# Optimization experiments

Measured on AMD Instinct MI355X. Metric: run time of the kernel, lower is better.

## Reference

```python
import jax, jax.numpy as jnp
import numpy as np

EPS = 1e-5


def conv1x1(x, w, b):
    # x: [b,c,h,w], w: [o,c], b: [o] -> [b,o,h,w]  (1x1 conv == channel matmul)
    return jnp.einsum('bchw,oc->bohw', x, w) + b[None, :, None, None]


def nor_mean_std(x):
    # instance norm over spatial dims (torch calc_mean_std uses unbiased var)
    mean = jnp.mean(x, axis=(2, 3), keepdims=True)
    var = jnp.var(x, axis=(2, 3), keepdims=True, ddof=1)
    return (x - mean) / jnp.sqrt(var + EPS)


def nor_mean(x):
    mean = jnp.mean(x, axis=(2, 3), keepdims=True)
    return x - mean, mean


def net(x, w1, b1, w2, b2):
    return conv1x1(jax.nn.relu(conv1x1(x, w1, b1)), w2, b2)


def setup_inputs() -> dict:
    key = jax.random.key(0)
    ks = jax.random.split(key, 8)
    B, C, H, W = 8, 256, 128, 128
    return {
        'content': jax.random.normal(ks[0], (B, C, H, W), jnp.float32),
        'style': jax.random.normal(ks[1], (B, C, H, W), jnp.float32),
        'w1': jax.random.normal(ks[2], (128, 256), jnp.float32) * 0.05,
        'b1': jax.random.normal(ks[3], (128,), jnp.float32) * 0.05,
        'w2': jax.random.normal(ks[4], (32, 128), jnp.float32) * 0.05,
        'b2': jax.random.normal(ks[5], (32,), jnp.float32) * 0.05,
        'wu': jax.random.normal(ks[6], (256, 32), jnp.float32) * 0.05,
        'bu': jax.random.normal(ks[7], (256,), jnp.float32) * 0.05,
    }


def reference(content, style, w1, b1, w2, b2, wu, bu):
    cF_nor = nor_mean_std(content)
    sF_nor, smean = nor_mean(style)
    cF = net(cF_nor, w1, b1, w2, b2)          # [b,32,h,w]
    sF = net(sF_nor, w1, b1, w2, b2)          # [b,32,h,w]
    b, c, h, w = cF.shape
    hw = h * w
    sf = sF.reshape(b, c, hw)
    # channel covariance: [b,32,32]
    s_cov = jnp.einsum('bcn,bdn->bcd', sf, sf) / hw
    s_cov = jax.nn.softmax(s_cov, axis=-1) * (c ** -0.5)
    gF = jnp.einsum('bcd,bdn->bcn', s_cov, cF.reshape(b, c, hw)).reshape(b, c, h, w)
    gF = conv1x1(gF, wu, bu)                  # [b,256,h,w]
    return gF + smean + content
```

## Files before the change

### kernel.cpp

```cpp
#include <hip/hip_runtime.h>

#define HW 16384
#define C_IN 256
#define C_MID 128
#define C_OUT 32
#define EPSF 1e-5f

typedef __bf16 bf16x8 __attribute__((ext_vector_type(8)));
typedef __bf16 bf16x4 __attribute__((ext_vector_type(4)));
typedef float f32x4 __attribute__((ext_vector_type(4)));

__global__ __launch_bounds__(512) void k_stats6(const float* __restrict__ content,
                                                const float* __restrict__ style,
                                                float* __restrict__ cmean,
                                                float* __restrict__ crstd,
                                                float* __restrict__ smean) {
    const int bc = blockIdx.x;
    const int t = threadIdx.x;
    const f32x4* cp = (const f32x4*)(content + (size_t)bc * HW);
    const f32x4* sp = (const f32x4*)(style + (size_t)bc * HW);
    const int phase = (bc * 257) & 4095;

    f32x4 c0 = __builtin_nontemporal_load(cp + ((phase + t          ) & 4095));
    f32x4 c1 = __builtin_nontemporal_load(cp + ((phase + t +  1*512) & 4095));
    f32x4 c2 = __builtin_nontemporal_load(cp + ((phase + t +  2*512) & 4095));
    f32x4 c3 = __builtin_nontemporal_load(cp + ((phase + t +  3*512) & 4095));
    f32x4 c4 = __builtin_nontemporal_load(cp + ((phase + t +  4*512) & 4095));
    f32x4 c5 = __builtin_nontemporal_load(cp + ((phase + t +  5*512) & 4095));
    f32x4 c6 = __builtin_nontemporal_load(cp + ((phase + t +  6*512) & 4095));
    f32x4 c7 = __builtin_nontemporal_load(cp + ((phase + t +  7*512) & 4095));
    f32x4 s0 = __builtin_nontemporal_load(sp + ((phase + t          ) & 4095));
    f32x4 s1 = __builtin_nontemporal_load(sp + ((phase + t +  1*512) & 4095));
    f32x4 s2 = __builtin_nontemporal_load(sp + ((phase + t +  2*512) & 4095));
    f32x4 s3 = __builtin_nontemporal_load(sp + ((phase + t +  3*512) & 4095));
    f32x4 s4 = __builtin_nontemporal_load(sp + ((phase + t +  4*512) & 4095));
    f32x4 s5 = __builtin_nontemporal_load(sp + ((phase + t +  5*512) & 4095));
    f32x4 s6 = __builtin_nontemporal_load(sp + ((phase + t +  6*512) & 4095));
    f32x4 s7 = __builtin_nontemporal_load(sp + ((phase + t +  7*512) & 4095));
    asm volatile("" ::
        "v"(c0), "v"(c1), "v"(c2), "v"(c3), "v"(c4), "v"(c5), "v"(c6), "v"(c7),
        "v"(s0), "v"(s1), "v"(s2), "v"(s3), "v"(s4), "v"(s5), "v"(s6), "v"(s7));

    float cs, cq, ss;
    {
        f32x4 a01 = c0 + c1, a23 = c2 + c3, a45 = c4 + c5, a67 = c6 + c7;
        f32x4 a = (a01 + a23) + (a45 + a67);
        cs = (a[0] + a[1]) + (a[2] + a[3]);
        f32x4 q01 = c0 * c0 + c1 * c1, q23 = c2 * c2 + c3 * c3;
        f32x4 q45 = c4 * c4 + c5 * c5, q67 = c6 * c6 + c7 * c7;
        f32x4 q = (q01 + q23) + (q45 + q67);
        cq = (q[0] + q[1]) + (q[2] + q[3]);
        f32x4 b01 = s0 + s1, b23 = s2 + s3, b45 = s4 + s5, b67 = s6 + s7;
        f32x4 bsum = (b01 + b23) + (b45 + b67);
        ss = (bsum[0] + bsum[1]) + (bsum[2] + bsum[3]);
    }

    #pragma unroll
    for (int d = 32; d > 0; d >>= 1) {
        cs += __shfl_xor(cs, d, 64);
        cq += __shfl_xor(cq, d, 64);
        ss += __shfl_xor(ss, d, 64);
    }
    __shared__ float rs[8], rq[8], rss[8];
    const int wv = t >> 6;
    if ((t & 63) == 0) { rs[wv] = cs; rq[wv] = cq; rss[wv] = ss; }
    __syncthreads();
    if (t == 0) {
        float S = 0.f, Q = 0.f, SS = 0.f;
        #pragma unroll
        for (int i = 0; i < 8; ++i) { S += rs[i]; Q += rq[i]; SS += rss[i]; }
        float n = (float)HW;
        float var = (Q - S * S / n) / (n - 1.f);
        cmean[bc] = S / n;
        crstd[bc] = 1.f / sqrtf(var + EPSF);
        smean[bc] = SS / n;
    }
}

__global__ __launch_bounds__(256) void k_wprep(const float* __restrict__ w1,
                                               const float* __restrict__ b1,
                                               const float* __restrict__ cmean,
                                               const float* __restrict__ crstd,
                                               const float* __restrict__ smean,
                                               __bf16* __restrict__ W1c,
                                               float* __restrict__ bias1c,
                                               __bf16* __restrict__ W1s,
                                               float* __restrict__ bias1s) {
    int o = blockIdx.x, b = blockIdx.y, t = threadIdx.x;
    float w = w1[o * 256 + t];
    float r = crstd[b * 256 + t];
    float wc = w * r;
    W1c[((size_t)(b * 128 + o)) * 256 + t] = (__bf16)wc;
    if (b == 0) W1s[o * 256 + t] = (__bf16)w;
    float pc = wc * cmean[b * 256 + t];
    float ps = w * smean[b * 256 + t];
    __shared__ float rA[256], rB[256];
    rA[t] = pc; rB[t] = ps;
    __syncthreads();
    for (int off = 128; off > 0; off >>= 1) {
        if (t < off) { rA[t] += rA[t + off]; rB[t] += rB[t + off]; }
        __syncthreads();
    }
    if (t == 0) {
        bias1c[b * 128 + o] = b1[o] - rA[0];
        bias1s[b * 128 + o] = b1[o] - rB[0];
    }
}

__global__ __launch_bounds__(256) void k_w2prep(const float* __restrict__ w2,
                                                __bf16* __restrict__ W2b) {
    int i = blockIdx.x * 256 + threadIdx.x;
    if (i < 4096) W2b[i] = (__bf16)w2[i];
}

__global__ __launch_bounds__(256) void k_net_mfma(const float* __restrict__ x,
                                                  const __bf16* __restrict__ W1,
                                                  const float* __restrict__ bias1,
                                                  const __bf16* __restrict__ W2,
                                                  const float* __restrict__ b2,
                                                  float* __restrict__ outF,
                                                  int w1_per_batch) {
    __shared__ __bf16 Xl[64 * 256];
    __shared__ __bf16 Tl[64 * 128];
    const int tid = threadIdx.x;
    const int l = tid & 63, wv = tid >> 6;
    const int lr = l & 15, g = l >> 4;
    const int sw = (lr & 7) << 4;
    const int p0 = blockIdx.x * 64;
    const int b = blockIdx.y;
    const float* xb = x + (size_t)b * C_IN * HW;

    {
        const int p = wv * 16 + lr;
        const float* xp = xb + p0 + p;
        char* row = (char*)&Xl[p * 256];
        #pragma unroll 4
        for (int cc = 0; cc < 16; ++cc) {
            const int c = cc * 16 + g * 4;
            float f0 = xp[(size_t)(c + 0) * HW];
            float f1 = xp[(size_t)(c + 1) * HW];
            float f2 = xp[(size_t)(c + 2) * HW];
            float f3 = xp[(size_t)(c + 3) * HW];
            bf16x4 v;
            v[0] = (__bf16)f0; v[1] = (__bf16)f1; v[2] = (__bf16)f2; v[3] = (__bf16)f3;
            *(bf16x4*)(row + ((c * 2) ^ sw)) = v;
        }
    }
    __syncthreads();

    const f32x4 zero4 = {0.f, 0.f, 0.f, 0.f};
    f32x4 acc[2][4];
    #pragma unroll
    for (int mt = 0; mt < 2; ++mt)
        #pragma unroll
        for (int nt = 0; nt < 4; ++nt) acc[mt][nt] = zero4;

    const __bf16* W1b = W1 + (w1_per_batch ? ((size_t)b << 15) : 0);
    const __bf16* wrow0 = W1b + (size_t)(wv * 32 + lr) * 256 + g * 8;
    const __bf16* wrow1 = wrow0 + 16 * 256;

    #pragma unroll
    for (int kt = 0; kt < 8; ++kt) {
        bf16x8 a0 = *(const bf16x8*)(wrow0 + kt * 32);
        bf16x8 a1 = *(const bf16x8*)(wrow1 + kt * 32);
        #pragma unroll
        for (int nt = 0; nt < 4; ++nt) {
            const char* xrow = (const char*)&Xl[(nt * 16 + lr) * 256];
            bf16x8 bfr = *(const bf16x8*)(xrow + (((kt * 32 + g * 8) * 2) ^ sw));
            acc[0][nt] = __builtin_amdgcn_mfma_f32_16x16x32_bf16(a0, bfr, acc[0][nt], 0, 0, 0);
            acc[1][nt] = __builtin_amdgcn_mfma_f32_16x16x32_bf16(a1, bfr, acc[1][nt], 0, 0, 0);
        }
    }

    float4 bia[2];
    bia[0] = *(const float4*)&bias1[b * 128 + wv * 32 + g * 4];
    bia[1] = *(const float4*)&bias1[b * 128 + wv * 32 + 16 + g * 4];
    #pragma unroll
    for (int mt = 0; mt < 2; ++mt) {
        #pragma unroll
        for (int nt = 0; nt < 4; ++nt) {
            const int p = nt * 16 + lr;
            char* trow = (char*)&Tl[p * 128];
            const int ob = (wv * 32 + mt * 16 + g * 4) * 2;
            bf16x4 tv;
            tv[0] = (__bf16)fmaxf(acc[mt][nt][0] + bia[mt].x, 0.f);
            tv[1] = (__bf16)fmaxf(acc[mt][nt][1] + bia[mt].y, 0.f);
            tv[2] = (__bf16)fmaxf(acc[mt][nt][2] + bia[mt].z, 0.f);
            tv[3] = (__bf16)fmaxf(acc[mt][nt][3] + bia[mt].w, 0.f);
            *(bf16x4*)(trow + (ob ^ sw)) = tv;
        }
    }
    __syncthreads();

    f32x4 acc2[2];
    acc2[0] = zero4; acc2[1] = zero4;
    const int p = wv * 16 + lr;
    const char* trow = (const char*)&Tl[p * 128];
    const __bf16* w2r0 = W2 + (size_t)lr * 128 + g * 8;
    const __bf16* w2r1 = w2r0 + 16 * 128;
    #pragma unroll
    for (int kt = 0; kt < 4; ++kt) {
        bf16x8 bfr = *(const bf16x8*)(trow + (((kt * 32 + g * 8) * 2) ^ sw));
        bf16x8 a0 = *(const bf16x8*)(w2r0 + kt * 32);
        bf16x8 a1 = *(const bf16x8*)(w2r1 + kt * 32);
        acc2[0] = __builtin_amdgcn_mfma_f32_16x16x32_bf16(a0, bfr, acc2[0], 0, 0, 0);
        acc2[1] = __builtin_amdgcn_mfma_f32_16x16x32_bf16(a1, bfr, acc2[1], 0, 0, 0);
    }
    float4 bb0 = *(const float4*)&b2[g * 4];
    float4 bb1 = *(const float4*)&b2[16 + g * 4];
    float* ob = outF + (size_t)b * C_OUT * HW + p0 + p;
    const int o0 = g * 4;
    ob[(size_t)(o0 + 0) * HW] = acc2[0][0] + bb0.x;
    ob[(size_t)(o0 + 1) * HW] = acc2[0][1] + bb0.y;
    ob[(size_t)(o0 + 2) * HW] = acc2[0][2] + bb0.z;
    ob[(size_t)(o0 + 3) * HW] = acc2[0][3] + bb0.w;
    ob[(size_t)(16 + o0 + 0) * HW] = acc2[1][0] + bb1.x;
    ob[(size_t)(16 + o0 + 1) * HW] = acc2[1][1] + bb1.y;
    ob[(size_t)(16 + o0 + 2) * HW] = acc2[1][2] + bb1.z;
    ob[(size_t)(16 + o0 + 3) * HW] = acc2[1][3] + bb1.w;
}

__global__ __launch_bounds__(256) void k_gram(const float* __restrict__ sF,
                                              float* __restrict__ partial) {
    __shared__ float sS[32 * 257];
    int b = blockIdx.y, sl = blockIdx.x;
    int t = threadIdx.x;
    const float* base = sF + (size_t)b * C_OUT * HW + sl * 1024;
    int i = t >> 3, jb = (t & 7) * 4;
    float acc[4] = {0.f, 0.f, 0.f, 0.f};
    for (int ch = 0; ch < 4; ++ch) {
        __syncthreads();
        #pragma unroll
        for (int r = 0; r < 32; ++r)
            sS[r * 257 + t] = base[(size_t)r * HW + ch * 256 + t];
        __syncthreads();
        for (int n = 0; n < 256; ++n) {
            float si = sS[i * 257 + n];
            #pragma unroll
            for (int q = 0; q < 4; ++q)
                acc[q] = fmaf(si, sS[(jb + q) * 257 + n], acc[q]);
        }
    }
    float* dst = partial + ((size_t)(b * 16 + sl)) * 1024 + t * 4;
    #pragma unroll
    for (int q = 0; q < 4; ++q) dst[q] = acc[q];
}

__global__ __launch_bounds__(1024) void k_softmax(const float* __restrict__ partial,
                                                  float* __restrict__ scov) {
    int b = blockIdx.x;
    int j = threadIdx.x, i = threadIdx.y;
    float v = 0.f;
    #pragma unroll
    for (int s = 0; s < 16; ++s)
        v += partial[((size_t)(b * 16 + s)) * 1024 + i * 32 + j];
    v *= (1.f / (float)HW);
    float m = v;
    #pragma unroll
    for (int d = 16; d > 0; d >>= 1) m = fmaxf(m, __shfl_xor(m, d, 32));
    float e = expf(v - m);
    float sum = e;
    #pragma unroll
    for (int d = 16; d > 0; d >>= 1) sum += __shfl_xor(sum, d, 32);
    scov[(size_t)b * 1024 + i * 32 + j] = e / sum * 0.17677669529663687f;
}

__global__ __launch_bounds__(256) void k_final(const float* __restrict__ cF,
                                               const float* __restrict__ scov,
                                               const float* __restrict__ wu,
                                               const float* __restrict__ bu,
                                               const float* __restrict__ smean,
                                               const float* __restrict__ content,
                                               float* __restrict__ out) {
    __shared__ float sCov[1024];
    __shared__ float sC[32 * 64];
    __shared__ float sG[32 * 64];
    __shared__ float sWu[32 * 260];
    int t = threadIdx.x;
    int p0 = blockIdx.x * 64;
    int b = blockIdx.y;
    #pragma unroll
    for (int q = 0; q < 4; ++q) sCov[t + 256 * q] = scov[(size_t)b * 1024 + t + 256 * q];
    {
        int p = t & 63, rb = t >> 6;
        #pragma unroll
        for (int pass = 0; pass < 8; ++pass) {
            int r = pass * 4 + rb;
            sC[r * 64 + p] = cF[(size_t)b * C_OUT * HW + (size_t)r * HW + p0 + p];
        }
    }
    {
        int k = t & 31, ob = t >> 5;
        #pragma unroll
        for (int pass = 0; pass < 32; ++pass) {
            int o = pass * 8 + ob;
            sWu[k * 260 + o] = wu[o * 32 + k];
        }
    }
    __syncthreads();
    {
        int gp = t & 63, gib = (t >> 6) * 8;
        #pragma unroll
        for (int rr = 0; rr < 8; ++rr) {
            int gi = gib + rr;
            float a = 0.f;
            #pragma unroll
            for (int k = 0; k < 32; ++k)
                a = fmaf(sCov[gi * 32 + k], sC[k * 64 + gp], a);
            sG[gi * 64 + gp] = a;
        }
    }
    __syncthreads();
    int tx = t & 7, ty = t >> 3;
    float acc[8][8];
    #pragma unroll
    for (int i = 0; i < 8; ++i)
        #pragma unroll
        for (int j = 0; j < 8; ++j) acc[i][j] = 0.f;
    #pragma unroll 4
    for (int k = 0; k < 32; ++k) {
        float4 a4a = *(const float4*)&sWu[k * 260 + ty * 8];
        float4 a4b = *(const float4*)&sWu[k * 260 + ty * 8 + 4];
        float4 b4a = *(const float4*)&sG[k * 64 + tx * 8];
        float4 b4b = *(const float4*)&sG[k * 64 + tx * 8 + 4];
        float a[8] = {a4a.x, a4a.y, a4a.z, a4a.w, a4b.x, a4b.y, a4b.z, a4b.w};
        float bb[8] = {b4a.x, b4a.y, b4a.z, b4a.w, b4b.x, b4b.y, b4b.z, b4b.w};
        #pragma unroll
        for (int i = 0; i < 8; ++i)
            #pragma unroll
            for (int j = 0; j < 8; ++j)
                acc[i][j] = fmaf(a[i], bb[j], acc[i][j]);
    }
    #pragma unroll
    for (int i = 0; i < 8; ++i) {
        int o = ty * 8 + i;
        float add = bu[o] + smean[b * 256 + o];
        const float* csrc = content + (size_t)b * C_IN * HW + (size_t)o * HW + p0 + tx * 8;
        float* dst = out + (size_t)b * C_IN * HW + (size_t)o * HW + p0 + tx * 8;
        float4 c0 = *(const float4*)csrc;
        float4 c1 = *(const float4*)(csrc + 4);
        f32x4 r0 = {acc[i][0] + add + c0.x, acc[i][1] + add + c0.y,
                    acc[i][2] + add + c0.z, acc[i][3] + add + c0.w};
        f32x4 r1 = {acc[i][4] + add + c1.x, acc[i][5] + add + c1.y,
                    acc[i][6] + add + c1.z, acc[i][7] + add + c1.w};
        __builtin_nontemporal_store(r0, (f32x4*)dst);
        __builtin_nontemporal_store(r1, (f32x4*)(dst + 4));
    }
}

extern "C" void kernel_launch(void* const* d_in, const int* in_sizes, int n_in,
                              void* d_out, int out_size, void* d_ws, size_t ws_size,
                              hipStream_t stream) {
    const float* content = (const float*)d_in[0];
    const float* style   = (const float*)d_in[1];
    const float* w1      = (const float*)d_in[2];
    const float* b1      = (const float*)d_in[3];
    const float* w2      = (const float*)d_in[4];
    const float* b2      = (const float*)d_in[5];
    const float* wu      = (const float*)d_in[6];
    const float* bu      = (const float*)d_in[7];
    float* out = (float*)d_out;
    float* ws  = (float*)d_ws;

    float* cmean   = ws;
    float* crstd   = ws + 2048;
    float* smean   = ws + 4096;
    float* scov    = ws + 6144;
    __bf16* W2b    = (__bf16*)(ws + 6144);
    float* bias1c  = ws + 8192;
    float* bias1s  = ws + 9216;
    float* partial = ws + 14336;
    __bf16* W1c    = (__bf16*)(ws + 14336);
    __bf16* W1s    = (__bf16*)(ws + 145408);
    float* cF      = ws + 161792;
    float* sF      = cF + 4194304;

    k_stats6<<<dim3(2048), 512, 0, stream>>>(content, style, cmean, crstd, smean);
    k_wprep<<<dim3(128, 8), 256, 0, stream>>>(w1, b1, cmean, crstd, smean,
                                              W1c, bias1c, W1s, bias1s);
    k_w2prep<<<dim3(16), 256, 0, stream>>>(w2, W2b);
    k_net_mfma<<<dim3(256, 8), 256, 0, stream>>>(content, W1c, bias1c, W2b, b2, cF, 1);
    k_net_mfma<<<dim3(256, 8), 256, 0, stream>>>(style, W1s, bias1s, W2b, b2, sF, 0);
    k_gram<<<dim3(16, 8), 256, 0, stream>>>(sF, partial);
    k_softmax<<<dim3(8), dim3(32, 32), 0, stream>>>(partial, scov);
    k_final<<<dim3(256, 8), 256, 0, stream>>>(cF, scov, wu, bu, smean, content, out);
}
```

Measured before the change: 261.8 us.

## Emit bf16 input copies in stats pass and fuse gram into style net

The statistics kernel now also writes bf16 copies of content and style. Both net kernels read these half-width copies instead of the fp32 tensors. The style net computes per-block Gram partials directly from LDS, which removes the sF buffer and the separate gram kernel, and the softmax then reduces 256 partials instead of 16. The w2 conversion is merged into the weight-prep kernel, the final kernel reads Wu straight from global memory, and the residual content is read from the bf16 copy. Together these cut HBM traffic and launch count, at the cost of extra bf16 writes and lower precision on the residual add.

New measurement: 245.4 us. -6.3%, faster.

```diff
diff --git a/kernel.cpp b/kernel.cpp
--- a/kernel.cpp
+++ b/kernel.cpp
@@ -10,47 +10,59 @@
 typedef __bf16 bf16x4 __attribute__((ext_vector_type(4)));
 typedef float f32x4 __attribute__((ext_vector_type(4)));
 
-__global__ __launch_bounds__(512) void k_stats6(const float* __restrict__ content,
-                                                const float* __restrict__ style,
-                                                float* __restrict__ cmean,
-                                                float* __restrict__ crstd,
-                                                float* __restrict__ smean) {
+__device__ __forceinline__ bf16x4 cvt4(f32x4 v) {
+    bf16x4 r;
+    r[0] = (__bf16)v[0]; r[1] = (__bf16)v[1];
+    r[2] = (__bf16)v[2]; r[3] = (__bf16)v[3];
+    return r;
+}
+
+__global__ __launch_bounds__(512) void k_stats10(const float* __restrict__ content,
+                                                 const float* __restrict__ style,
+                                                 float* __restrict__ cmean,
+                                                 float* __restrict__ crstd,
+                                                 float* __restrict__ smean,
+                                                 __bf16* __restrict__ cbf,
+                                                 __bf16* __restrict__ sbf) {
     const int bc = blockIdx.x;
     const int t = threadIdx.x;
     const f32x4* cp = (const f32x4*)(content + (size_t)bc * HW);
     const f32x4* sp = (const f32x4*)(style + (size_t)bc * HW);
     const int phase = (bc * 257) & 4095;
 
-    f32x4 c0 = __builtin_nontemporal_load(cp + ((phase + t          ) & 4095));
-    f32x4 c1 = __builtin_nontemporal_load(cp + ((phase + t +  1*512) & 4095));
-    f32x4 c2 = __builtin_nontemporal_load(cp + ((phase + t +  2*512) & 4095));
-    f32x4 c3 = __builtin_nontemporal_load(cp + ((phase + t +  3*512) & 4095));
-    f32x4 c4 = __builtin_nontemporal_load(cp + ((phase + t +  4*512) & 4095));
-    f32x4 c5 = __builtin_nontemporal_load(cp + ((phase + t +  5*512) & 4095));
-    f32x4 c6 = __builtin_nontemporal_load(cp + ((phase + t +  6*512) & 4095));
-    f32x4 c7 = __builtin_nontemporal_load(cp + ((phase + t +  7*512) & 4095));
-    f32x4 s0 = __builtin_nontemporal_load(sp + ((phase + t          ) & 4095));
-    f32x4 s1 = __builtin_nontemporal_load(sp + ((phase + t +  1*512) & 4095));
-    f32x4 s2 = __builtin_nontemporal_load(sp + ((phase + t +  2*512) & 4095));
-    f32x4 s3 = __builtin_nontemporal_load(sp + ((phase + t +  3*512) & 4095));
-    f32x4 s4 = __builtin_nontemporal_load(sp + ((phase + t +  4*512) & 4095));
-    f32x4 s5 = __builtin_nontemporal_load(sp + ((phase + t +  5*512) & 4095));
-    f32x4 s6 = __builtin_nontemporal_load(sp + ((phase + t +  6*512) & 4095));
-    f32x4 s7 = __builtin_nontemporal_load(sp + ((phase + t +  7*512) & 4095));
+    int idx[8];
+    #pragma unroll
+    for (int i = 0; i < 8; ++i) idx[i] = (phase + t + i * 512) & 4095;
+
+    f32x4 c[8], s[8];
+    #pragma unroll
+    for (int i = 0; i < 8; ++i) c[i] = __builtin_nontemporal_load(cp + idx[i]);
+    #pragma unroll
+    for (int i = 0; i < 8; ++i) s[i] = __builtin_nontemporal_load(sp + idx[i]);
     asm volatile("" ::
-        "v"(c0), "v"(c1), "v"(c2), "v"(c3), "v"(c4), "v"(c5), "v"(c6), "v"(c7),
-        "v"(s0), "v"(s1), "v"(s2), "v"(s3), "v"(s4), "v"(s5), "v"(s6), "v"(s7));
+        "v"(c[0]), "v"(c[1]), "v"(c[2]), "v"(c[3]), "v"(c[4]), "v"(c[5]), "v"(c[6]), "v"(c[7]),
+        "v"(s[0]), "v"(s[1]), "v"(s[2]), "v"(s[3]), "v"(s[4]), "v"(s[5]), "v"(s[6]), "v"(s[7]));
+
+    {
+        bf16x4* cb = (bf16x4*)(cbf + (size_t)bc * HW);
+        bf16x4* sb = (bf16x4*)(sbf + (size_t)bc * HW);
+        #pragma unroll
+        for (int i = 0; i < 8; ++i) {
+            cb[idx[i]] = cvt4(c[i]);
+            sb[idx[i]] = cvt4(s[i]);
+        }
+    }
 
     float cs, cq, ss;
     {
-        f32x4 a01 = c0 + c1, a23 = c2 + c3, a45 = c4 + c5, a67 = c6 + c7;
+        f32x4 a01 = c[0] + c[1], a23 = c[2] + c[3], a45 = c[4] + c[5], a67 = c[6] + c[7];
         f32x4 a = (a01 + a23) + (a45 + a67);
         cs = (a[0] + a[1]) + (a[2] + a[3]);
-        f32x4 q01 = c0 * c0 + c1 * c1, q23 = c2 * c2 + c3 * c3;
-        f32x4 q45 = c4 * c4 + c5 * c5, q67 = c6 * c6 + c7 * c7;
+        f32x4 q01 = c[0]*c[0] + c[1]*c[1], q23 = c[2]*c[2] + c[3]*c[3];
+        f32x4 q45 = c[4]*c[4] + c[5]*c[5], q67 = c[6]*c[6] + c[7]*c[7];
         f32x4 q = (q01 + q23) + (q45 + q67);
         cq = (q[0] + q[1]) + (q[2] + q[3]);
-        f32x4 b01 = s0 + s1, b23 = s2 + s3, b45 = s4 + s5, b67 = s6 + s7;
+        f32x4 b01 = s[0] + s[1], b23 = s[2] + s[3], b45 = s[4] + s[5], b67 = s[6] + s[7];
         f32x4 bsum = (b01 + b23) + (b45 + b67);
         ss = (bsum[0] + bsum[1]) + (bsum[2] + bsum[3]);
     }
@@ -77,21 +89,26 @@
     }
 }
 
-__global__ __launch_bounds__(256) void k_wprep(const float* __restrict__ w1,
-                                               const float* __restrict__ b1,
-                                               const float* __restrict__ cmean,
-                                               const float* __restrict__ crstd,
-                                               const float* __restrict__ smean,
-                                               __bf16* __restrict__ W1c,
-                                               float* __restrict__ bias1c,
-                                               __bf16* __restrict__ W1s,
-                                               float* __restrict__ bias1s) {
+__global__ __launch_bounds__(256) void k_wprep2(const float* __restrict__ w1,
+                                                const float* __restrict__ b1,
+                                                const float* __restrict__ w2,
+                                                const float* __restrict__ cmean,
+                                                const float* __restrict__ crstd,
+                                                const float* __restrict__ smean,
+                                                __bf16* __restrict__ W1c,
+                                                float* __restrict__ bias1c,
+                                                __bf16* __restrict__ W1s,
+                                                float* __restrict__ bias1s,
+                                                __bf16* __restrict__ W2b) {
     int o = blockIdx.x, b = blockIdx.y, t = threadIdx.x;
     float w = w1[o * 256 + t];
     float r = crstd[b * 256 + t];
     float wc = w * r;
     W1c[((size_t)(b * 128 + o)) * 256 + t] = (__bf16)wc;
-    if (b == 0) W1s[o * 256 + t] = (__bf16)w;
+    if (b == 0) {
+        W1s[o * 256 + t] = (__bf16)w;
+        if (t < 32) W2b[o * 32 + t] = (__bf16)w2[o * 32 + t];
+    }
     float pc = wc * cmean[b * 256 + t];
     float ps = w * smean[b * 256 + t];
     __shared__ float rA[256], rB[256];
@@ -107,19 +124,15 @@
     }
 }
 
-__global__ __launch_bounds__(256) void k_w2prep(const float* __restrict__ w2,
-                                                __bf16* __restrict__ W2b) {
-    int i = blockIdx.x * 256 + threadIdx.x;
-    if (i < 4096) W2b[i] = (__bf16)w2[i];
-}
-
-__global__ __launch_bounds__(256) void k_net_mfma(const float* __restrict__ x,
-                                                  const __bf16* __restrict__ W1,
-                                                  const float* __restrict__ bias1,
-                                                  const __bf16* __restrict__ W2,
-                                                  const float* __restrict__ b2,
-                                                  float* __restrict__ outF,
-                                                  int w1_per_batch) {
+template <int MODE>
+__global__ __launch_bounds__(256) void k_net_bf(const __bf16* __restrict__ x,
+                                                const __bf16* __restrict__ W1,
+                                                const float* __restrict__ bias1,
+                                                const __bf16* __restrict__ W2,
+                                                const float* __restrict__ b2,
+                                                float* __restrict__ outF,
+                                                float* __restrict__ partial,
+                                                int w1_per_batch) {
     __shared__ __bf16 Xl[64 * 256];
     __shared__ __bf16 Tl[64 * 128];
     const int tid = threadIdx.x;
@@ -128,21 +141,20 @@
     const int sw = (lr & 7) << 4;
     const int p0 = blockIdx.x * 64;
     const int b = blockIdx.y;
-    const float* xb = x + (size_t)b * C_IN * HW;
+    const __bf16* xb = x + (size_t)b * C_IN * HW;
 
     {
         const int p = wv * 16 + lr;
-        const float* xp = xb + p0 + p;
+        const __bf16* xp = xb + p0 + p;
         char* row = (char*)&Xl[p * 256];
         #pragma unroll 4
         for (int cc = 0; cc < 16; ++cc) {
             const int c = cc * 16 + g * 4;
-            float f0 = xp[(size_t)(c + 0) * HW];
-            float f1 = xp[(size_t)(c + 1) * HW];
-            float f2 = xp[(size_t)(c + 2) * HW];
-            float f3 = xp[(size_t)(c + 3) * HW];
             bf16x4 v;
-            v[0] = (__bf16)f0; v[1] = (__bf16)f1; v[2] = (__bf16)f2; v[3] = (__bf16)f3;
+            v[0] = xp[(size_t)(c + 0) * HW];
+            v[1] = xp[(size_t)(c + 1) * HW];
+            v[2] = xp[(size_t)(c + 2) * HW];
+            v[3] = xp[(size_t)(c + 3) * HW];
             *(bf16x4*)(row + ((c * 2) ^ sw)) = v;
         }
     }
@@ -175,6 +187,7 @@
     float4 bia[2];
     bia[0] = *(const float4*)&bias1[b * 128 + wv * 32 + g * 4];
     bia[1] = *(const float4*)&bias1[b * 128 + wv * 32 + 16 + g * 4];
+    __syncthreads();
     #pragma unroll
     for (int mt = 0; mt < 2; ++mt) {
         #pragma unroll
@@ -208,53 +221,58 @@
     }
     float4 bb0 = *(const float4*)&b2[g * 4];
     float4 bb1 = *(const float4*)&b2[16 + g * 4];
-    float* ob = outF + (size_t)b * C_OUT * HW + p0 + p;
     const int o0 = g * 4;
-    ob[(size_t)(o0 + 0) * HW] = acc2[0][0] + bb0.x;
-    ob[(size_t)(o0 + 1) * HW] = acc2[0][1] + bb0.y;
-    ob[(size_t)(o0 + 2) * HW] = acc2[0][2] + bb0.z;
-    ob[(size_t)(o0 + 3) * HW] = acc2[0][3] + bb0.w;
-    ob[(size_t)(16 + o0 + 0) * HW] = acc2[1][0] + bb1.x;
-    ob[(size_t)(16 + o0 + 1) * HW] = acc2[1][1] + bb1.y;
-    ob[(size_t)(16 + o0 + 2) * HW] = acc2[1][2] + bb1.z;
-    ob[(size_t)(16 + o0 + 3) * HW] = acc2[1][3] + bb1.w;
-}
-
-__global__ __launch_bounds__(256) void k_gram(const float* __restrict__ sF,
-                                              float* __restrict__ partial) {
-    __shared__ float sS[32 * 257];
-    int b = blockIdx.y, sl = blockIdx.x;
-    int t = threadIdx.x;
-    const float* base = sF + (size_t)b * C_OUT * HW + sl * 1024;
-    int i = t >> 3, jb = (t & 7) * 4;
-    float acc[4] = {0.f, 0.f, 0.f, 0.f};
-    for (int ch = 0; ch < 4; ++ch) {
+
+    if constexpr (MODE == 0) {
+        float* ob = outF + (size_t)b * C_OUT * HW + p0 + p;
+        ob[(size_t)(o0 + 0) * HW] = acc2[0][0] + bb0.x;
+        ob[(size_t)(o0 + 1) * HW] = acc2[0][1] + bb0.y;
+        ob[(size_t)(o0 + 2) * HW] = acc2[0][2] + bb0.z;
+        ob[(size_t)(o0 + 3) * HW] = acc2[0][3] + bb0.w;
+        ob[(size_t)(16 + o0 + 0) * HW] = acc2[1][0] + bb1.x;
+        ob[(size_t)(16 + o0 + 1) * HW] = acc2[1][1] + bb1.y;
+        ob[(size_t)(16 + o0 + 2) * HW] = acc2[1][2] + bb1.z;
+        ob[(size_t)(16 + o0 + 3) * HW] = acc2[1][3] + bb1.w;
+    } else {
+        float* gt = (float*)Xl;
+        gt[(o0 + 0) * 65 + p] = acc2[0][0] + bb0.x;
+        gt[(o0 + 1) * 65 + p] = acc2[0][1] + bb0.y;
+        gt[(o0 + 2) * 65 + p] = acc2[0][2] + bb0.z;
+        gt[(o0 + 3) * 65 + p] = acc2[0][3] + bb0.w;
+        gt[(16 + o0 + 0) * 65 + p] = acc2[1][0] + bb1.x;
+        gt[(16 + o0 + 1) * 65 + p] = acc2[1][1] + bb1.y;
+        gt[(16 + o0 + 2) * 65 + p] = acc2[1][2] + bb1.z;
+        gt[(16 + o0 + 3) * 65 + p] = acc2[1][3] + bb1.w;
         __syncthreads();
-        #pragma unroll
-        for (int r = 0; r < 32; ++r)
-            sS[r * 257 + t] = base[(size_t)r * HW + ch * 256 + t];
-        __syncthreads();
-        for (int n = 0; n < 256; ++n) {
-            float si = sS[i * 257 + n];
+        const int gi = tid >> 3, jb = (tid & 7) * 4;
+        float g4[4] = {0.f, 0.f, 0.f, 0.f};
+        #pragma unroll 8
+        for (int n = 0; n < 64; ++n) {
+            float si = gt[gi * 65 + n];
             #pragma unroll
             for (int q = 0; q < 4; ++q)
-                acc[q] = fmaf(si, sS[(jb + q) * 257 + n], acc[q]);
-        }
-    }
-    float* dst = partial + ((size_t)(b * 16 + sl)) * 1024 + t * 4;
-    #pragma unroll
-    for (int q = 0; q < 4; ++q) dst[q] = acc[q];
-}
-
-__global__ __launch_bounds__(1024) void k_softmax(const float* __restrict__ partial,
-                                                  float* __restrict__ scov) {
+                g4[q] = fmaf(si, gt[(jb + q) * 65 + n], g4[q]);
+        }
+        float* dst = partial + ((size_t)(b * 256 + blockIdx.x)) * 1024 + tid * 4;
+        #pragma unroll
+        for (int q = 0; q < 4; ++q) dst[q] = g4[q];
+    }
+}
+
+__global__ __launch_bounds__(1024) void k_softmax2(const float* __restrict__ partial,
+                                                   float* __restrict__ scov) {
     int b = blockIdx.x;
     int j = threadIdx.x, i = threadIdx.y;
-    float v = 0.f;
-    #pragma unroll
-    for (int s = 0; s < 16; ++s)
-        v += partial[((size_t)(b * 16 + s)) * 1024 + i * 32 + j];
-    v *= (1.f / (float)HW);
+    const float* base = partial + (size_t)b * 256 * 1024 + i * 32 + j;
+    float v0 = 0.f, v1 = 0.f, v2 = 0.f, v3 = 0.f;
+    #pragma unroll 4
+    for (int s = 0; s < 256; s += 4) {
+        v0 += base[(s + 0) * 1024];
+        v1 += base[(s + 1) * 1024];
+        v2 += base[(s + 2) * 1024];
+        v3 += base[(s + 3) * 1024];
+    }
+    float v = ((v0 + v1) + (v2 + v3)) * (1.f / (float)HW);
     float m = v;
     #pragma unroll
     for (int d = 16; d > 0; d >>= 1) m = fmaxf(m, __shfl_xor(m, d, 32));
@@ -265,17 +283,16 @@
     scov[(size_t)b * 1024 + i * 32 + j] = e / sum * 0.17677669529663687f;
 }
 
-__global__ __launch_bounds__(256) void k_final(const float* __restrict__ cF,
-                                               const float* __restrict__ scov,
-                                               const float* __restrict__ wu,
-                                               const float* __restrict__ bu,
-                                               const float* __restrict__ smean,
-                                               const float* __restrict__ content,
-                                               float* __restrict__ out) {
+__global__ __launch_bounds__(256) void k_final3(const float* __restrict__ cF,
+                                                const float* __restrict__ scov,
+                                                const float* __restrict__ wu,
+                                                const float* __restrict__ bu,
+                                                const float* __restrict__ smean,
+                                                const __bf16* __restrict__ cbf,
+                                                float* __restrict__ out) {
     __shared__ float sCov[1024];
     __shared__ float sC[32 * 64];
     __shared__ float sG[32 * 64];
-    __shared__ float sWu[32 * 260];
     int t = threadIdx.x;
     int p0 = blockIdx.x * 64;
     int b = blockIdx.y;
@@ -287,14 +304,6 @@
         for (int pass = 0; pass < 8; ++pass) {
             int r = pass * 4 + rb;
             sC[r * 64 + p] = cF[(size_t)b * C_OUT * HW + (size_t)r * HW + p0 + p];
-        }
-    }
-    {
-        int k = t & 31, ob = t >> 5;
-        #pragma unroll
-        for (int pass = 0; pass < 32; ++pass) {
-            int o = pass * 8 + ob;
-            sWu[k * 260 + o] = wu[o * 32 + k];
         }
     }
     __syncthreads();
@@ -312,6 +321,7 @@
     }
     __syncthreads();
     int tx = t & 7, ty = t >> 3;
+    const float* wurow = wu + (size_t)(ty * 8) * 32;
     float acc[8][8];
     #pragma unroll
     for (int i = 0; i < 8; ++i)
@@ -319,11 +329,11 @@
         for (int j = 0; j < 8; ++j) acc[i][j] = 0.f;
     #pragma unroll 4
     for (int k = 0; k < 32; ++k) {
-        float4 a4a = *(const float4*)&sWu[k * 260 + ty * 8];
-        float4 a4b = *(const float4*)&sWu[k * 260 + ty * 8 + 4];
+        float a[8];
+        #pragma unroll
+        for (int i = 0; i < 8; ++i) a[i] = wurow[i * 32 + k];
         float4 b4a = *(const float4*)&sG[k * 64 + tx * 8];
         float4 b4b = *(const float4*)&sG[k * 64 + tx * 8 + 4];
-        float a[8] = {a4a.x, a4a.y, a4a.z, a4a.w, a4b.x, a4b.y, a4b.z, a4b.w};
         float bb[8] = {b4a.x, b4a.y, b4a.z, b4a.w, b4b.x, b4b.y, b4b.z, b4b.w};
         #pragma unroll
         for (int i = 0; i < 8; ++i)
@@ -335,14 +345,13 @@
     for (int i = 0; i < 8; ++i) {
         int o = ty * 8 + i;
         float add = bu[o] + smean[b * 256 + o];
-        const float* csrc = content + (size_t)b * C_IN * HW + (size_t)o * HW + p0 + tx * 8;
+        const __bf16* csrc = cbf + (size_t)b * C_IN * HW + (size_t)o * HW + p0 + tx * 8;
         float* dst = out + (size_t)b * C_IN * HW + (size_t)o * HW + p0 + tx * 8;
-        float4 c0 = *(const float4*)csrc;
-        float4 c1 = *(const float4*)(csrc + 4);
-        f32x4 r0 = {acc[i][0] + add + c0.x, acc[i][1] + add + c0.y,
-                    acc[i][2] + add + c0.z, acc[i][3] + add + c0.w};
-        f32x4 r1 = {acc[i][4] + add + c1.x, acc[i][5] + add + c1.y,
-                    acc[i][6] + add + c1.z, acc[i][7] + add + c1.w};
+        bf16x8 cvv = *(const bf16x8*)csrc;
+        f32x4 r0 = {acc[i][0] + add + (float)cvv[0], acc[i][1] + add + (float)cvv[1],
+                    acc[i][2] + add + (float)cvv[2], acc[i][3] + add + (float)cvv[3]};
+        f32x4 r1 = {acc[i][4] + add + (float)cvv[4], acc[i][5] + add + (float)cvv[5],
+                    acc[i][6] + add + (float)cvv[6], acc[i][7] + add + (float)cvv[7]};
         __builtin_nontemporal_store(r0, (f32x4*)dst);
         __builtin_nontemporal_store(r1, (f32x4*)(dst + 4));
     }
@@ -366,22 +375,21 @@
     float* crstd   = ws + 2048;
     float* smean   = ws + 4096;
     float* scov    = ws + 6144;
-    __bf16* W2b    = (__bf16*)(ws + 6144);
-    float* bias1c  = ws + 8192;
-    float* bias1s  = ws + 9216;
-    float* partial = ws + 14336;
-    __bf16* W1c    = (__bf16*)(ws + 14336);
-    __bf16* W1s    = (__bf16*)(ws + 145408);
-    float* cF      = ws + 161792;
-    float* sF      = cF + 4194304;
-
-    k_stats6<<<dim3(2048), 512, 0, stream>>>(content, style, cmean, crstd, smean);
-    k_wprep<<<dim3(128, 8), 256, 0, stream>>>(w1, b1, cmean, crstd, smean,
-                                              W1c, bias1c, W1s, bias1s);
-    k_w2prep<<<dim3(16), 256, 0, stream>>>(w2, W2b);
-    k_net_mfma<<<dim3(256, 8), 256, 0, stream>>>(content, W1c, bias1c, W2b, b2, cF, 1);
-    k_net_mfma<<<dim3(256, 8), 256, 0, stream>>>(style, W1s, bias1s, W2b, b2, sF, 0);
-    k_gram<<<dim3(16, 8), 256, 0, stream>>>(sF, partial);
-    k_softmax<<<dim3(8), dim3(32, 32), 0, stream>>>(partial, scov);
-    k_final<<<dim3(256, 8), 256, 0, stream>>>(cF, scov, wu, bu, smean, content, out);
-}
+    float* bias1c  = ws + 14336;
+    float* bias1s  = ws + 15360;
+    __bf16* W2b    = (__bf16*)(ws + 16384);
+    __bf16* W1s    = (__bf16*)(ws + 18432);
+    __bf16* W1c    = (__bf16*)(ws + 34816);
+    float* partial = ws + 165888;
+    float* cF      = ws + 2263040;
+    __bf16* cbf    = (__bf16*)(ws + 6457344);
+    __bf16* sbf    = (__bf16*)(ws + 23234560);
+
+    k_stats10<<<dim3(2048), 512, 0, stream>>>(content, style, cmean, crstd, smean, cbf, sbf);
+    k_wprep2<<<dim3(128, 8), 256, 0, stream>>>(w1, b1, w2, cmean, crstd, smean,
+                                               W1c, bias1c, W1s, bias1s, W2b);
+    k_net_bf<0><<<dim3(256, 8), 256, 0, stream>>>(cbf, W1c, bias1c, W2b, b2, cF, nullptr, 1);
+    k_net_bf<1><<<dim3(256, 8), 256, 0, stream>>>(sbf, W1s, bias1s, W2b, b2, nullptr, partial, 0);
+    k_softmax2<<<dim3(8), dim3(32, 32), 0, stream>>>(partial, scov);
+    k_final3<<<dim3(256, 8), 256, 0, stream>>>(cF, scov, wu, bu, smean, cbf, out);
+}
```
